# Optimization experiments

Measured on AMD Instinct MI355X. Metric: run time of the kernel, lower is better.

The kernel has to match this reference:

```python
import jax, jax.numpy as jnp
import numpy as np

N_MB = 4  # number of micro-behavior buckets; C = N_MB**2 + 1

def setup_inputs() -> dict:
    key = jax.random.key(0)
    k_q, k_k, k_b, k_w, k_a = jax.random.split(key, 5)
    b, h, S, d = 8, 8, 512, 64
    C = N_MB * N_MB + 1
    return {
        "query": jax.random.normal(k_q, (b, h, S, d), dtype=jnp.float32),
        "key": jax.random.normal(k_k, (b, h, S, d), dtype=jnp.float32),
        "b_seq": jax.random.randint(k_b, (b, S), 0, N_MB + 1, dtype=jnp.int32),
        "W1": jax.random.normal(k_w, (N_MB, h, d, d), dtype=jnp.float32) * 0.02,
        "alpha1": jax.random.normal(k_a, (C, N_MB, h), dtype=jnp.float32) * 0.02,
    }

def reference(query, key, b_seq, W1, alpha1):
    # bucket-pair index per (i, j) token pair; 0 if either token is padding
    bi = b_seq[:, :, None]  # [b, S, 1]
    bj = b_seq[:, None, :]  # [b, 1, S]
    b_mat = ((bi - 1) * N_MB + bj) * (bi * bj != 0).astype(jnp.int32)  # [b, S, S]
    # mix the n_mb base bilinear weights into C per-bucket-pair matrices
    W1_ = jnp.einsum('Bhmn,CBh->Chmn', W1, jax.nn.softmax(alpha1, axis=1))
    # full bilinear score for every bucket-pair class C (the wasteful part)
    att_all = jnp.einsum('bhim,Chmn,bhjn->bhijC', query, W1_, key)  # [b,h,S,S,C]
    # select the score matching each pair's bucket index
    idx = b_mat[:, None, :, :, None].astype(jnp.int32)  # [b,1,S,S,1] -> broadcast over h
    idx = jnp.broadcast_to(idx, att_all.shape[:4] + (1,))
    scores = jnp.take_along_axis(att_all, idx, axis=4)[..., 0]  # [b,h,S,S]
    return scores
```

## Files before the change

kernel.cpp:

```cpp
#include <hip/hip_runtime.h>
#include <stdint.h>

#define NB 4
#define NC 17
#define HH 8
#define SS 512
#define DD 64
#define CT 64

typedef __attribute__((ext_vector_type(8))) short bf16x8;
typedef __attribute__((ext_vector_type(4))) float f32x4;

#define WS_W1   0
#define WS_RIDX 1114112
#define WS_GST  (WS_RIDX + 16384)

__device__ __forceinline__ unsigned short f2bf(float f) {
  unsigned int x; __builtin_memcpy(&x, &f, 4);
  return (unsigned short)((x + 0x7fff + ((x >> 16) & 1)) >> 16);
}
__device__ __forceinline__ bf16x8 cvt8(float4 a, float4 b) {
  union { bf16x8 v; unsigned short u[8]; } t;
  t.u[0] = f2bf(a.x); t.u[1] = f2bf(a.y); t.u[2] = f2bf(a.z); t.u[3] = f2bf(a.w);
  t.u[4] = f2bf(b.x); t.u[5] = f2bf(b.y); t.u[6] = f2bf(b.z); t.u[7] = f2bf(b.w);
  return t.v;
}

__global__ __launch_bounds__(256) void k_prep(const int* __restrict__ bseq,
                                              const float* __restrict__ W1,
                                              const float* __restrict__ alpha,
                                              int* __restrict__ ridx,
                                              int* __restrict__ gst,
                                              unsigned short* __restrict__ W1mbf) {
  int tid = threadIdx.x;
  if (blockIdx.x < 8) {
    int b = blockIdx.x;
    __shared__ int cnt[5], base[6], cur[5];
    if (tid < 5) cnt[tid] = 0;
    __syncthreads();
    for (int j = tid; j < SS; j += blockDim.x) atomicAdd(&cnt[bseq[b * SS + j]], 1);
    __syncthreads();
    if (tid == 0) {
      base[0] = 0;
      for (int k = 0; k < 5; k++) base[k + 1] = base[k] + cnt[k];
      for (int k = 0; k < 6; k++) gst[b * 6 + k] = base[k];
    }
    __syncthreads();
    if (tid < 5) cur[tid] = base[tid];
    __syncthreads();
    for (int j = tid; j < SS; j += blockDim.x) {
      int p = atomicAdd(&cur[bseq[b * SS + j]], 1);
      ridx[b * SS + p] = j;
    }
  } else {
    int cb = blockIdx.x - 8;
    int c = cb >> 3, hh = cb & 7;
    __shared__ float sm[NB];
    if (tid == 0) {
      float a[NB], mx = -1e30f;
      for (int B = 0; B < NB; B++) { a[B] = alpha[(c * NB + B) * HH + hh]; mx = fmaxf(mx, a[B]); }
      float s = 0.f;
      for (int B = 0; B < NB; B++) { a[B] = __expf(a[B] - mx); s += a[B]; }
      for (int B = 0; B < NB; B++) sm[B] = a[B] / s;
    }
    __syncthreads();
    float s0 = sm[0], s1 = sm[1], s2 = sm[2], s3 = sm[3];
    const float* w0p = &W1[((0 * HH + hh) << 12)];
    const float* w1p = &W1[((1 * HH + hh) << 12)];
    const float* w2p = &W1[((2 * HH + hh) << 12)];
    const float* w3p = &W1[((3 * HH + hh) << 12)];
    unsigned short* dst = &W1mbf[((size_t)(c * HH + hh)) << 12];
    for (int idx = tid * 4; idx < DD * DD; idx += 1024) {
      float4 w0 = *(const float4*)(w0p + idx);
      float4 w1 = *(const float4*)(w1p + idx);
      float4 w2 = *(const float4*)(w2p + idx);
      float4 w3 = *(const float4*)(w3p + idx);
      union { unsigned short u[4]; uint2 v; } o;
      o.u[0] = f2bf(w0.x * s0 + w1.x * s1 + w2.x * s2 + w3.x * s3);
      o.u[1] = f2bf(w0.y * s0 + w1.y * s1 + w2.y * s2 + w3.y * s3);
      o.u[2] = f2bf(w0.z * s0 + w1.z * s1 + w2.z * s2 + w3.z * s3);
      o.u[3] = f2bf(w0.w * s0 + w1.w * s1 + w2.w * s2 + w3.w * s3);
      *(uint2*)(dst + idx) = o.v;
    }
  }
}

__global__ __launch_bounds__(768, 6) void k_fused(const float* __restrict__ query,
                                                  const float* __restrict__ key,
                                                  const int* __restrict__ bseq,
                                                  const unsigned short* __restrict__ W1mbf,
                                                  const int* __restrict__ ridx,
                                                  const int* __restrict__ gst,
                                                  float* __restrict__ out) {
  int bx = blockIdx.x;
  int bh = bx & 63, jt = bx >> 6;
  int b = bh >> 3, h = bh & 7;
  int j0 = jt * CT;
  int tid = threadIdx.x, wave = tid >> 6, lane = tid & 63;
  int quad = lane >> 4, l16 = lane & 15;

  __shared__ __align__(16) unsigned short Tl[5][CT][72];
  __shared__ int ord[CT];
  __shared__ int ridxs[SS];
  __shared__ int p1list[40], p2list[40];
  __shared__ int n1tot, n2tot;

  if (tid < SS) ridxs[tid] = ridx[b * SS + tid];

  if (wave == 0) {
    int mybj = bseq[b * SS + j0 + lane];
    unsigned long long mm[5];
    int pb[6];
    pb[0] = 0;
#pragma unroll
    for (int a = 0; a < 5; a++) {
      mm[a] = __ballot(mybj == a);
      pb[a + 1] = pb[a] + (int)__popcll(mm[a]);
    }
    int pos = pb[mybj] + (int)__popcll(mm[mybj] & ((1ull << lane) - 1ull));
    ord[pos] = lane;

    int n1b_[5]; int t = 0;
#pragma unroll
    for (int a = 0; a < 5; a++) {
      n1b_[a] = t;
      t += ((pb[a + 1] - pb[a] + 15) >> 4) * ((a == 0) ? 1 : 5);
    }
    if (lane == 0) n1tot = t;

    if (lane < 5) {
      int a = lane;
      int ls = pb[a], le = pb[a + 1];
      int w = n1b_[a];
      for (int t0 = ls; t0 < le; t0 += 16) {
        if (a == 0) {
          p1list[w++] = t0 | (le << 6) | (1 << 21);
        } else {
#pragma unroll
          for (int B = 0; B < 5; B++) {
            int c = (B == 0) ? 0 : (B - 1) * NB + a;
            p1list[w++] = t0 | (le << 6) | (c << 13) | (B << 18);
          }
        }
      }
      int g[6];
#pragma unroll
      for (int k = 0; k < 6; k++) g[k] = gst[b * 6 + k];
      int w2 = 0;
      for (int aa = 0; aa < a; aa++) w2 += (g[aa + 1] - g[aa] + 15) >> 4;
      int gs = g[a], ge = g[a + 1];
      for (int p0 = gs; p0 < ge; p0 += 16)
        p2list[w2++] = p0 | (ge << 10) | (a << 20);
      if (a == 4) n2tot = w2;
    }
  }
  __syncthreads();

  for (int idx = wave; idx < n1tot; idx += 12) {
    int e = p1list[idx];
    int t0 = e & 63, le = (e >> 6) & 127, c = (e >> 13) & 31, B = (e >> 18) & 7;
    int bc = (e >> 21) & 1;
    const unsigned short* Wc = W1mbf + ((size_t)(c * HH + h) << 12);
    int p = t0 + l16; if (p > le - 1) p = le - 1;
    int cl = ord[p];
    const float* kp = &key[((size_t)(bh * SS + j0 + cl)) * DD + quad * 8];
    float4 ka = *(const float4*)kp, kb = *(const float4*)(kp + 4);
    float4 kc = *(const float4*)(kp + 32), kd = *(const float4*)(kp + 36);
    bf16x8 af0 = cvt8(ka, kb);
    bf16x8 af1 = cvt8(kc, kd);
    int cr[4];
#pragma unroll
    for (int reg = 0; reg < 4; reg++) {
      int pr = t0 + quad * 4 + reg;
      cr[reg] = (pr < le) ? ord[pr] : -1;
    }
    f32x4 acc[4];
#pragma unroll
    for (int nt = 0; nt < 4; nt++) {
      const unsigned short* wp = &Wc[(l16 * 4 + nt) * DD + quad * 8];
      bf16x8 b0 = *(const bf16x8*)wp;
      bf16x8 b1 = *(const bf16x8*)(wp + 32);
      f32x4 z = {0.f, 0.f, 0.f, 0.f};
      __builtin_amdgcn_s_setprio(1);
      z = __builtin_amdgcn_mfma_f32_16x16x32_bf16(af0, b0, z, 0, 0, 0);
      z = __builtin_amdgcn_mfma_f32_16x16x32_bf16(af1, b1, z, 0, 0, 0);
      __builtin_amdgcn_s_setprio(0);
      acc[nt] = z;
    }
#pragma unroll
    for (int reg = 0; reg < 4; reg++) {
      if (cr[reg] >= 0) {
        union { unsigned short u[4]; uint2 v; } o;
        o.u[0] = f2bf(acc[0][reg]); o.u[1] = f2bf(acc[1][reg]);
        o.u[2] = f2bf(acc[2][reg]); o.u[3] = f2bf(acc[3][reg]);
        if (bc) {
#pragma unroll
          for (int Bw = 0; Bw < 5; Bw++) *(uint2*)&Tl[Bw][cr[reg]][l16 * 4] = o.v;
        } else {
          *(uint2*)&Tl[B][cr[reg]][l16 * 4] = o.v;
        }
      }
    }
  }
  __syncthreads();

  for (int i0 = wave * 2; i0 < n2tot; i0 += 24) {
    int e0 = p2list[i0];
    bool has1 = (i0 + 1) < n2tot;
    int e1 = has1 ? p2list[i0 + 1] : e0;

    int p0a = e0 & 1023, gea = (e0 >> 10) & 1023, Ba = e0 >> 20;
    int p0b = e1 & 1023, geb = (e1 >> 10) & 1023, Bb = e1 >> 20;

    int pa = p0a + l16; if (pa > gea - 1) pa = gea - 1;
    int ra = ridxs[pa];
    const float* qa = &query[((size_t)(bh * SS + ra)) * DD + quad * 8];
    float4 a0 = *(const float4*)qa, a1 = *(const float4*)(qa + 4);
    float4 a2 = *(const float4*)(qa + 32), a3 = *(const float4*)(qa + 36);
    bf16x8 afa0 = cvt8(a0, a1), afa1 = cvt8(a2, a3);

    int pb_ = p0b + l16; if (pb_ > geb - 1) pb_ = geb - 1;
    int rb = ridxs[pb_];
    const float* qb = &query[((size_t)(bh * SS + rb)) * DD + quad * 8];
    float4 b0_ = *(const float4*)qb, b1_ = *(const float4*)(qb + 4);
    float4 b2_ = *(const float4*)(qb + 32), b3_ = *(const float4*)(qb + 36);
    bf16x8 afb0 = cvt8(b0_, b1_), afb1 = cvt8(b2_, b3_);

    int rra[4], rrb[4];
#pragma unroll
    for (int reg = 0; reg < 4; reg++) {
      int pra = p0a + quad * 4 + reg;
      rra[reg] = (pra < gea) ? ridxs[pra] : -1;
      int prb = p0b + quad * 4 + reg;
      rrb[reg] = (has1 && prb < geb) ? ridxs[prb] : -1;
    }

    f32x4 acca[4], accb[4];
#pragma unroll
    for (int ct = 0; ct < 4; ct++) {
      const unsigned short* tpa = &Tl[Ba][l16 * 4 + ct][quad * 8];
      const unsigned short* tpb = &Tl[Bb][l16 * 4 + ct][quad * 8];
      bf16x8 ba0 = *(const bf16x8*)tpa;
      bf16x8 ba1 = *(const bf16x8*)(tpa + 32);
      bf16x8 bb0 = *(const bf16x8*)tpb;
      bf16x8 bb1 = *(const bf16x8*)(tpb + 32);
      f32x4 za = {0.f, 0.f, 0.f, 0.f}, zb = {0.f, 0.f, 0.f, 0.f};
      __builtin_amdgcn_s_setprio(1);
      za = __builtin_amdgcn_mfma_f32_16x16x32_bf16(afa0, ba0, za, 0, 0, 0);
      zb = __builtin_amdgcn_mfma_f32_16x16x32_bf16(afb0, bb0, zb, 0, 0, 0);
      za = __builtin_amdgcn_mfma_f32_16x16x32_bf16(afa1, ba1, za, 0, 0, 0);
      zb = __builtin_amdgcn_mfma_f32_16x16x32_bf16(afb1, bb1, zb, 0, 0, 0);
      __builtin_amdgcn_s_setprio(0);
      acca[ct] = za; accb[ct] = zb;
    }
#pragma unroll
    for (int reg = 0; reg < 4; reg++) {
      if (rra[reg] >= 0) {
        f32x4 v = {acca[0][reg], acca[1][reg], acca[2][reg], acca[3][reg]};
        __builtin_nontemporal_store(v,
            (f32x4*)&out[((size_t)(bh * SS + rra[reg])) * SS + j0 + l16 * 4]);
      }
      if (rrb[reg] >= 0) {
        f32x4 v = {accb[0][reg], accb[1][reg], accb[2][reg], accb[3][reg]};
        __builtin_nontemporal_store(v,
            (f32x4*)&out[((size_t)(bh * SS + rrb[reg])) * SS + j0 + l16 * 4]);
      }
    }
  }
}

extern "C" void kernel_launch(void* const* d_in, const int* in_sizes, int n_in,
                              void* d_out, int out_size, void* d_ws, size_t ws_size,
                              hipStream_t stream) {
  const float* q = (const float*)d_in[0];
  const float* k = (const float*)d_in[1];
  const int* bseq = (const int*)d_in[2];
  const float* W1 = (const float*)d_in[3];
  const float* alpha = (const float*)d_in[4];
  float* out = (float*)d_out;
  char* ws = (char*)d_ws;
  unsigned short* W1mbf = (unsigned short*)(ws + WS_W1);
  int* ridx = (int*)(ws + WS_RIDX);
  int* gst = (int*)(ws + WS_GST);

  hipLaunchKernelGGL(k_prep, dim3(8 + NC * HH), dim3(256), 0, stream,
                     bseq, W1, alpha, ridx, gst, W1mbf);
  hipLaunchKernelGGL(k_fused, dim3(64 * (SS / CT)), dim3(768), 0, stream,
                     q, k, bseq, W1mbf, ridx, gst, out);
}
```

Before: 115.3 us.

## Prefetch first phase-2 query tile before phase 1 and XOR-swizzle the shared T tile

Each wave now issues the global loads for its first phase-2 query rows before the phase-1 key×W MFMA loop, so their latency hides behind phase-1 work and the barrier. The shared Tl buffer is also addressed through an XOR swizzle on the byte column, keyed by row, to reduce LDS bank conflicts on the strided row reads in phase 2. The prefetched float4 registers stay live across phase 1, which raises register pressure and may lower occupancy.

```diff
diff --git a/kernel.cpp b/kernel.cpp
--- a/kernel.cpp
+++ b/kernel.cpp
@@ -105,6 +105,10 @@
   __shared__ int p1list[40], p2list[40];
   __shared__ int n1tot, n2tot;
 
+#define TLP(Bp, rowp, colByte) \
+  ((unsigned short*)((char*)Tl + (((Bp) * CT + (rowp)) * 144) + \
+                     ((colByte) ^ ((((rowp) >> 2) & 7) << 4))))
+
   if (tid < SS) ridxs[tid] = ridx[b * SS + tid];
 
   if (wave == 0) {
@@ -155,6 +159,26 @@
     }
   }
   __syncthreads();
+
+  float4 A0, A1, A2, A3, A4, A5, A6, A7;
+  int pe0, pe1; bool phas1;
+  {
+    int pi = wave * 2;
+    bool ph = pi < n2tot;
+    pe0 = ph ? p2list[pi] : (1 << 10);
+    phas1 = ph && (pi + 1) < n2tot;
+    pe1 = phas1 ? p2list[pi + 1] : pe0;
+    int p0a = pe0 & 1023, gea = (pe0 >> 10) & 1023;
+    int pa = p0a + l16; if (pa > gea - 1) pa = gea - 1;
+    const float* qa = &query[((size_t)(bh * SS + ridxs[pa])) * DD + quad * 8];
+    A0 = *(const float4*)qa; A1 = *(const float4*)(qa + 4);
+    A2 = *(const float4*)(qa + 32); A3 = *(const float4*)(qa + 36);
+    int p0b = pe1 & 1023, geb = (pe1 >> 10) & 1023;
+    int pb2 = p0b + l16; if (pb2 > geb - 1) pb2 = geb - 1;
+    const float* qb = &query[((size_t)(bh * SS + ridxs[pb2])) * DD + quad * 8];
+    A4 = *(const float4*)qb; A5 = *(const float4*)(qb + 4);
+    A6 = *(const float4*)(qb + 32); A7 = *(const float4*)(qb + 36);
+  }
 
   for (int idx = wave; idx < n1tot; idx += 12) {
     int e = p1list[idx];
@@ -195,37 +219,22 @@
         o.u[2] = f2bf(acc[2][reg]); o.u[3] = f2bf(acc[3][reg]);
         if (bc) {
 #pragma unroll
-          for (int Bw = 0; Bw < 5; Bw++) *(uint2*)&Tl[Bw][cr[reg]][l16 * 4] = o.v;
+          for (int Bw = 0; Bw < 5; Bw++) *(uint2*)TLP(Bw, cr[reg], l16 * 8) = o.v;
         } else {
-          *(uint2*)&Tl[B][cr[reg]][l16 * 4] = o.v;
+          *(uint2*)TLP(B, cr[reg], l16 * 8) = o.v;
         }
       }
     }
   }
   __syncthreads();
 
-  for (int i0 = wave * 2; i0 < n2tot; i0 += 24) {
-    int e0 = p2list[i0];
-    bool has1 = (i0 + 1) < n2tot;
-    int e1 = has1 ? p2list[i0 + 1] : e0;
-
+  auto p2body = [&](int e0, int e1, bool has1,
+                    float4 a0, float4 a1, float4 a2, float4 a3,
+                    float4 b0_, float4 b1_, float4 b2_, float4 b3_) {
     int p0a = e0 & 1023, gea = (e0 >> 10) & 1023, Ba = e0 >> 20;
     int p0b = e1 & 1023, geb = (e1 >> 10) & 1023, Bb = e1 >> 20;
-
-    int pa = p0a + l16; if (pa > gea - 1) pa = gea - 1;
-    int ra = ridxs[pa];
-    const float* qa = &query[((size_t)(bh * SS + ra)) * DD + quad * 8];
-    float4 a0 = *(const float4*)qa, a1 = *(const float4*)(qa + 4);
-    float4 a2 = *(const float4*)(qa + 32), a3 = *(const float4*)(qa + 36);
     bf16x8 afa0 = cvt8(a0, a1), afa1 = cvt8(a2, a3);
-
-    int pb_ = p0b + l16; if (pb_ > geb - 1) pb_ = geb - 1;
-    int rb = ridxs[pb_];
-    const float* qb = &query[((size_t)(bh * SS + rb)) * DD + quad * 8];
-    float4 b0_ = *(const float4*)qb, b1_ = *(const float4*)(qb + 4);
-    float4 b2_ = *(const float4*)(qb + 32), b3_ = *(const float4*)(qb + 36);
     bf16x8 afb0 = cvt8(b0_, b1_), afb1 = cvt8(b2_, b3_);
-
     int rra[4], rrb[4];
 #pragma unroll
     for (int reg = 0; reg < 4; reg++) {
@@ -234,16 +243,14 @@
       int prb = p0b + quad * 4 + reg;
       rrb[reg] = (has1 && prb < geb) ? ridxs[prb] : -1;
     }
-
     f32x4 acca[4], accb[4];
 #pragma unroll
     for (int ct = 0; ct < 4; ct++) {
-      const unsigned short* tpa = &Tl[Ba][l16 * 4 + ct][quad * 8];
-      const unsigned short* tpb = &Tl[Bb][l16 * 4 + ct][quad * 8];
-      bf16x8 ba0 = *(const bf16x8*)tpa;
-      bf16x8 ba1 = *(const bf16x8*)(tpa + 32);
-      bf16x8 bb0 = *(const bf16x8*)tpb;
-      bf16x8 bb1 = *(const bf16x8*)(tpb + 32);
+      int rA = l16 * 4 + ct;
+      bf16x8 ba0 = *(const bf16x8*)TLP(Ba, rA, quad * 16);
+      bf16x8 ba1 = *(const bf16x8*)TLP(Ba, rA, 64 + quad * 16);
+      bf16x8 bb0 = *(const bf16x8*)TLP(Bb, rA, quad * 16);
+      bf16x8 bb1 = *(const bf16x8*)TLP(Bb, rA, 64 + quad * 16);
       f32x4 za = {0.f, 0.f, 0.f, 0.f}, zb = {0.f, 0.f, 0.f, 0.f};
       __builtin_amdgcn_s_setprio(1);
       za = __builtin_amdgcn_mfma_f32_16x16x32_bf16(afa0, ba0, za, 0, 0, 0);
@@ -266,7 +273,29 @@
             (f32x4*)&out[((size_t)(bh * SS + rrb[reg])) * SS + j0 + l16 * 4]);
       }
     }
-  }
+  };
+
+  int i0 = wave * 2;
+  if (i0 < n2tot) {
+    p2body(pe0, pe1, phas1, A0, A1, A2, A3, A4, A5, A6, A7);
+    for (i0 += 24; i0 < n2tot; i0 += 24) {
+      int e0 = p2list[i0];
+      bool has1 = (i0 + 1) < n2tot;
+      int e1 = has1 ? p2list[i0 + 1] : e0;
+      int p0a = e0 & 1023, gea = (e0 >> 10) & 1023;
+      int pa = p0a + l16; if (pa > gea - 1) pa = gea - 1;
+      const float* qa = &query[((size_t)(bh * SS + ridxs[pa])) * DD + quad * 8];
+      float4 a0 = *(const float4*)qa, a1 = *(const float4*)(qa + 4);
+      float4 a2 = *(const float4*)(qa + 32), a3 = *(const float4*)(qa + 36);
+      int p0b = e1 & 1023, geb = (e1 >> 10) & 1023;
+      int pb2 = p0b + l16; if (pb2 > geb - 1) pb2 = geb - 1;
+      const float* qb = &query[((size_t)(bh * SS + ridxs[pb2])) * DD + quad * 8];
+      float4 b0_ = *(const float4*)qb, b1_ = *(const float4*)(qb + 4);
+      float4 b2_ = *(const float4*)(qb + 32), b3_ = *(const float4*)(qb + 36);
+      p2body(e0, e1, has1, a0, a1, a2, a3, b0_, b1_, b2_, b3_);
+    }
+  }
+#undef TLP
 }
 
 extern "C" void kernel_launch(void* const* d_in, const int* in_sizes, int n_in,
```

After: 122.1 us (median of 2 runs). +5.9%, slower.
